# Kernel tuning notes

Hardware: AMD Instinct MI355X
Metric: run time of the kernel (lower is better)

Reference implementation:

```python
import jax, jax.numpy as jnp
import numpy as np

H = 32  # hidden_size from LSTMConfig

def setup_inputs() -> dict:
    key = jax.random.key(0)
    ks = jax.random.split(key, 7)
    B, T, F = 131072, 22, 12
    s = 1.0 / np.sqrt(H)
    return {
        "x": jax.random.normal(ks[0], (B, T, F), dtype=jnp.float32),
        "W_ih": jax.random.uniform(ks[1], (4 * H, F), minval=-s, maxval=s, dtype=jnp.float32),
        "W_hh": jax.random.uniform(ks[2], (4 * H, H), minval=-s, maxval=s, dtype=jnp.float32),
        "b_ih": jax.random.uniform(ks[3], (4 * H,), minval=-s, maxval=s, dtype=jnp.float32),
        "b_hh": jax.random.uniform(ks[4], (4 * H,), minval=-s, maxval=s, dtype=jnp.float32),
        "W_head": jax.random.uniform(ks[5], (1, H), minval=-s, maxval=s, dtype=jnp.float32),
        "b_head": jax.random.uniform(ks[6], (1,), minval=-s, maxval=s, dtype=jnp.float32),
    }

def _lstm_last_hidden(x, W_ih, W_hh, b_ih, b_hh):
    B, T, F = x.shape
    # precompute input contribution for all timesteps: [T, B, 4H]
    gx = jnp.einsum('btf,gf->tbg', x, W_ih) + (b_ih + b_hh)

    def step(carry, gx_t):
        h, c = carry
        g = gx_t + h @ W_hh.T                      # [B, 4H]
        i, f, gg, o = jnp.split(g, 4, axis=-1)     # PyTorch gate order i,f,g,o
        i = jax.nn.sigmoid(i)
        f = jax.nn.sigmoid(f)
        gg = jnp.tanh(gg)
        o = jax.nn.sigmoid(o)
        c = f * c + i * gg
        h = o * jnp.tanh(c)
        return (h, c), None

    h0 = jnp.zeros((B, H), dtype=x.dtype)
    (h, _), _ = jax.lax.scan(step, (h0, h0), gx)
    return h  # [B, H] last timestep hidden

def reference(x, W_ih, W_hh, b_ih, b_hh, W_head, b_head):
    h = _lstm_last_hidden(x, W_ih, W_hh, b_ih, b_hh)
    # Dropout p=0.0 is identity; Linear(H,1) + Softplus, then squeeze(-1)
    y = h @ W_head.T + b_head                      # [B, 1]
    return jax.nn.softplus(y)[:, 0]                # [B]
```

## Files before the change

### kernel.cpp

```cpp
#include <hip/hip_runtime.h>
#include <math.h>

#define T_STEPS 22
#define F_IN    12
#define HID     32

typedef __attribute__((ext_vector_type(8))) short  bf16x8;
typedef __attribute__((ext_vector_type(4)))  float f32x4;
typedef __attribute__((ext_vector_type(2)))  float f32x2;

union FragU { unsigned int u[4]; bf16x8 v; };

#define LOG2E    1.442695041f
#define TWOLOG2E 2.885390082f

static __device__ __forceinline__ unsigned short f2bf(float x) {
    unsigned int u = __builtin_bit_cast(unsigned int, x);
    return (unsigned short)((u + 0x7fffu + ((u >> 16) & 1u)) >> 16);
}

static __device__ __forceinline__ unsigned cvt_pk_bf16(float lo, float hi) {
    unsigned r;
    asm("v_cvt_pk_bf16_f32 %0, %1, %2" : "=v"(r) : "v"(lo), "v"(hi));
    return r;
}

__global__ void prep_kernel(const float* __restrict__ Wih, const float* __restrict__ Whh,
                            const float* __restrict__ bih, const float* __restrict__ bhh,
                            const float* __restrict__ Whead, float* __restrict__ ws) {
    const int tid = threadIdx.x;
    unsigned short* wx = (unsigned short*)ws;
    unsigned short* wh = (unsigned short*)(ws + 2048);
    float* whd = ws + 4096;

    for (int e = tid; e < 512; e += 256) {
        int tile = e >> 6, lane = e & 63;
        int row = lane & 15, s = lane >> 4;
        int g = 16 * tile + row;
        float scale = (tile == 4 || tile == 5) ? TWOLOG2E : -LOG2E;
        for (int j = 0; j < 8; ++j) {
            int k = 8 * s + j;
            float v = 0.0f;
            if (k < F_IN)       v = Wih[g * F_IN + k];
            else if (k == F_IN) v = bih[g] + bhh[g];
            wx[e * 8 + j] = f2bf(scale * v);
            int cc = (j < 4) ? (4 * s + j) : (16 + 4 * s + (j - 4));
            wh[e * 8 + j] = f2bf(scale * Whh[g * HID + cc]);
        }
    }
    if (tid < 32) {
        int s = tid >> 3, j = tid & 7;
        int orig = (j < 4) ? (4 * s + j) : (16 + 4 * s + (j - 4));
        whd[tid] = Whead[orig];
    }
}

__global__ void __launch_bounds__(256, 2)
lstm_kernel(const float* __restrict__ x, const float* __restrict__ ws,
            const float* __restrict__ bheadp, float* __restrict__ out, int B) {
    const int tid  = threadIdx.x;
    const int lane = tid & 63;
    const int wave = tid >> 6;
    const int col  = lane & 15;
    const int s    = lane >> 4;
    int b = blockIdx.x * 64 + wave * 16 + col;
    const bool valid = (b < B);
    if (b >= B) b = B - 1;

    __shared__ float wlds[4096];
#pragma unroll
    for (int i = 0; i < 4; ++i)
        ((float4*)wlds)[tid + i * 256] = ((const float4*)ws)[tid + i * 256];
    __syncthreads();

    const bf16x8* wx_l = (const bf16x8*)wlds;
    const bf16x8* wh_l = ((const bf16x8*)wlds) + 512;

    const float* xr  = x + (size_t)b * (T_STEPS * F_IN);
    const float* xa  = xr + ((s == 0) ? 0 : 8);
    const float* xbp = xr + ((s == 0) ? 4 : 8);

    f32x2 cc[4], hv[4];
#pragma unroll
    for (int q = 0; q < 4; ++q) { cc[q] = (f32x2){0.f, 0.f}; hv[q] = (f32x2){0.f, 0.f}; }
    bf16x8 hf;
#pragma unroll
    for (int j = 0; j < 8; ++j) hf[j] = 0;

    f32x4 zc;
#pragma unroll
    for (int q = 0; q < 4; ++q) zc[q] = 0.0f;

#pragma unroll 1
    for (int t = 0; t < T_STEPS; ++t) {
        asm volatile("" ::: "memory");

        float4 va = *(const float4*)(xa  + t * F_IN);
        float4 vb = *(const float4*)(xbp + t * F_IN);
        unsigned p0 = cvt_pk_bf16(va.x, va.y);
        unsigned p1 = cvt_pk_bf16(va.z, va.w);
        unsigned p2 = cvt_pk_bf16(vb.x, vb.y);
        unsigned p3 = cvt_pk_bf16(vb.z, vb.w);
        FragU xf;
        if (s == 0)      { xf.u[0] = p0; xf.u[1] = p1; xf.u[2] = p2;          xf.u[3] = p3; }
        else if (s == 1) { xf.u[0] = p0; xf.u[1] = p1; xf.u[2] = 0x00003f80u; xf.u[3] = 0;  }
        else             { xf.u[0] = 0;  xf.u[1] = 0;  xf.u[2] = 0;           xf.u[3] = 0;  }

        f32x4 a0, a1, a2, a3, a4, a5, a6, a7;
        a0 = __builtin_amdgcn_mfma_f32_16x16x32_bf16(wx_l[0 * 64 + lane], xf.v, zc, 0, 0, 0);
        a1 = __builtin_amdgcn_mfma_f32_16x16x32_bf16(wx_l[1 * 64 + lane], xf.v, zc, 0, 0, 0);
        a2 = __builtin_amdgcn_mfma_f32_16x16x32_bf16(wx_l[2 * 64 + lane], xf.v, zc, 0, 0, 0);
        a3 = __builtin_amdgcn_mfma_f32_16x16x32_bf16(wx_l[3 * 64 + lane], xf.v, zc, 0, 0, 0);
        a4 = __builtin_amdgcn_mfma_f32_16x16x32_bf16(wx_l[4 * 64 + lane], xf.v, zc, 0, 0, 0);
        a5 = __builtin_amdgcn_mfma_f32_16x16x32_bf16(wx_l[5 * 64 + lane], xf.v, zc, 0, 0, 0);
        a6 = __builtin_amdgcn_mfma_f32_16x16x32_bf16(wx_l[6 * 64 + lane], xf.v, zc, 0, 0, 0);
        a7 = __builtin_amdgcn_mfma_f32_16x16x32_bf16(wx_l[7 * 64 + lane], xf.v, zc, 0, 0, 0);
        a0 = __builtin_amdgcn_mfma_f32_16x16x32_bf16(wh_l[0 * 64 + lane], hf, a0, 0, 0, 0);
        a1 = __builtin_amdgcn_mfma_f32_16x16x32_bf16(wh_l[1 * 64 + lane], hf, a1, 0, 0, 0);
        a2 = __builtin_amdgcn_mfma_f32_16x16x32_bf16(wh_l[2 * 64 + lane], hf, a2, 0, 0, 0);
        a3 = __builtin_amdgcn_mfma_f32_16x16x32_bf16(wh_l[3 * 64 + lane], hf, a3, 0, 0, 0);
        a4 = __builtin_amdgcn_mfma_f32_16x16x32_bf16(wh_l[4 * 64 + lane], hf, a4, 0, 0, 0);
        a5 = __builtin_amdgcn_mfma_f32_16x16x32_bf16(wh_l[5 * 64 + lane], hf, a5, 0, 0, 0);
        a6 = __builtin_amdgcn_mfma_f32_16x16x32_bf16(wh_l[6 * 64 + lane], hf, a6, 0, 0, 0);
        a7 = __builtin_amdgcn_mfma_f32_16x16x32_bf16(wh_l[7 * 64 + lane], hf, a7, 0, 0, 0);
        __builtin_amdgcn_sched_group_barrier(0x100, 8, 0);
        __builtin_amdgcn_sched_group_barrier(0x008, 8, 0);
        __builtin_amdgcn_sched_group_barrier(0x100, 8, 0);
        __builtin_amdgcn_sched_group_barrier(0x008, 8, 0);

        const f32x2 one2 = {1.0f, 1.0f};
#pragma unroll
        for (int q = 0; q < 4; ++q) {
            f32x2 ei = {__builtin_amdgcn_exp2f(a0[q]), __builtin_amdgcn_exp2f(a1[q])};
            f32x2 ef = {__builtin_amdgcn_exp2f(a2[q]), __builtin_amdgcn_exp2f(a3[q])};
            f32x2 eg = {__builtin_amdgcn_exp2f(a4[q]), __builtin_amdgcn_exp2f(a5[q])};
            f32x2 eo = {__builtin_amdgcn_exp2f(a6[q]), __builtin_amdgcn_exp2f(a7[q])};
            f32x2 A  = (one2 + ei) * (one2 + eg);
            f32x2 F  = one2 + ef;
            f32x2 FA = F * A;
            f32x2 r1 = {__builtin_amdgcn_rcpf(FA.x), __builtin_amdgcn_rcpf(FA.y)};
            f32x2 t2 = eg * (f32x2){TWOLOG2E, TWOLOG2E} - (f32x2){TWOLOG2E, TWOLOG2E};
            f32x2 num = t2 * F + cc[q] * A;
            cc[q] = num * r1;
            f32x2 ec = {__builtin_amdgcn_exp2f(cc[q].x), __builtin_amdgcn_exp2f(cc[q].y)};
            f32x2 r2in = (one2 + eo) * (one2 + ec);
            f32x2 r2 = {__builtin_amdgcn_rcpf(r2in.x), __builtin_amdgcn_rcpf(r2in.y)};
            hv[q] = (ec - one2) * r2;
        }

        FragU hh;
        hh.u[0] = cvt_pk_bf16(hv[0].x, hv[1].x);
        hh.u[1] = cvt_pk_bf16(hv[2].x, hv[3].x);
        hh.u[2] = cvt_pk_bf16(hv[0].y, hv[1].y);
        hh.u[3] = cvt_pk_bf16(hv[2].y, hv[3].y);
        hf = hh.v;
    }

    const float* whd = ws + 4096 + s * 8;
    float y = 0.0f;
#pragma unroll
    for (int j = 0; j < 4; ++j) {
        y = fmaf(hv[j].x, whd[j],     y);
        y = fmaf(hv[j].y, whd[4 + j], y);
    }
    y += __shfl_xor(y, 16, 64);
    y += __shfl_xor(y, 32, 64);
    y += bheadp[0];
    float sp = fmaxf(y, 0.0f) + log1pf(expf(-fabsf(y)));
    if (valid && s == 0) out[b] = sp;
}

extern "C" void kernel_launch(void* const* d_in, const int* in_sizes, int n_in,
                              void* d_out, int out_size, void* d_ws, size_t ws_size,
                              hipStream_t stream) {
    const float* x     = (const float*)d_in[0];
    const float* Wih   = (const float*)d_in[1];
    const float* Whh   = (const float*)d_in[2];
    const float* bih   = (const float*)d_in[3];
    const float* bhh   = (const float*)d_in[4];
    const float* Whead = (const float*)d_in[5];
    const float* bhead = (const float*)d_in[6];
    float* out = (float*)d_out;
    float* ws  = (float*)d_ws;

    const int B = in_sizes[0] / (T_STEPS * F_IN);
    const int blocks = (B + 63) / 64;

    hipLaunchKernelGGL(prep_kernel, dim3(1), dim3(256), 0, stream,
                       Wih, Whh, bih, bhh, Whead, ws);
    hipLaunchKernelGGL(lstm_kernel, dim3(blocks), dim3(256), 0, stream,
                       x, ws, bhead, out, B);
}
```

Measured before the change: 103.4 us.

## Interleave two independent batch tiles per wave to hide MFMA and transcendental latency

Each wave now processes two 16-sample tiles, with two independent recurrence chains whose MFMA and exp/rcp work can overlap. Block size in samples doubles, so the grid is halved. Launch bounds are raised to 4 waves per SIMD. The sched_group_barrier hints are removed, and the head projection now reads the bf16-rounded hidden state instead of the fp32 values. This adds register pressure and a slight change in precision at the output.

```diff
diff --git a/kernel.cpp b/kernel.cpp
--- a/kernel.cpp
+++ b/kernel.cpp
@@ -23,6 +23,10 @@
     unsigned r;
     asm("v_cvt_pk_bf16_f32 %0, %1, %2" : "=v"(r) : "v"(lo), "v"(hi));
     return r;
+}
+
+static __device__ __forceinline__ float bf2f(short s_) {
+    return __builtin_bit_cast(float, ((unsigned)(unsigned short)s_) << 16);
 }
 
 __global__ void prep_kernel(const float* __restrict__ Wih, const float* __restrict__ Whh,
@@ -50,12 +54,13 @@
     }
     if (tid < 32) {
         int s = tid >> 3, j = tid & 7;
-        int orig = (j < 4) ? (4 * s + j) : (16 + 4 * s + (j - 4));
+        int orig = (j < 4) ? (4 * s + j) : (16 + 4 * s + (j - 8) + 4);
+        orig = (j < 4) ? (4 * s + j) : (16 + 4 * s + (j - 4));
         whd[tid] = Whead[orig];
     }
 }
 
-__global__ void __launch_bounds__(256, 2)
+__global__ void __launch_bounds__(256, 4)
 lstm_kernel(const float* __restrict__ x, const float* __restrict__ ws,
             const float* __restrict__ bheadp, float* __restrict__ out, int B) {
     const int tid  = threadIdx.x;
@@ -63,9 +68,12 @@
     const int wave = tid >> 6;
     const int col  = lane & 15;
     const int s    = lane >> 4;
-    int b = blockIdx.x * 64 + wave * 16 + col;
-    const bool valid = (b < B);
-    if (b >= B) b = B - 1;
+    const int base = blockIdx.x * 128 + wave * 32;
+    int b0 = base + col;
+    int b1 = base + 16 + col;
+    const bool v0 = (b0 < B), v1 = (b1 < B);
+    if (b0 >= B) b0 = B - 1;
+    if (b1 >= B) b1 = B - 1;
 
     __shared__ float wlds[4096];
 #pragma unroll
@@ -73,101 +81,168 @@
         ((float4*)wlds)[tid + i * 256] = ((const float4*)ws)[tid + i * 256];
     __syncthreads();
 
-    const bf16x8* wx_l = (const bf16x8*)wlds;
-    const bf16x8* wh_l = ((const bf16x8*)wlds) + 512;
-
-    const float* xr  = x + (size_t)b * (T_STEPS * F_IN);
-    const float* xa  = xr + ((s == 0) ? 0 : 8);
-    const float* xbp = xr + ((s == 0) ? 4 : 8);
-
-    f32x2 cc[4], hv[4];
-#pragma unroll
-    for (int q = 0; q < 4; ++q) { cc[q] = (f32x2){0.f, 0.f}; hv[q] = (f32x2){0.f, 0.f}; }
-    bf16x8 hf;
-#pragma unroll
-    for (int j = 0; j < 8; ++j) hf[j] = 0;
+    const int off1 = (s == 0) ? 0 : 8;
+    const int off2 = (s == 0) ? 4 : 8;
+    const float* xa0 = x + (size_t)b0 * (T_STEPS * F_IN) + off1;
+    const float* xb0 = x + (size_t)b0 * (T_STEPS * F_IN) + off2;
+    const float* xa1 = x + (size_t)b1 * (T_STEPS * F_IN) + off1;
+    const float* xb1 = x + (size_t)b1 * (T_STEPS * F_IN) + off2;
+
+    f32x2 cA[4], cB[4];
+#pragma unroll
+    for (int q = 0; q < 4; ++q) { cA[q] = (f32x2){0.f, 0.f}; cB[q] = (f32x2){0.f, 0.f}; }
+    bf16x8 hfA, hfB;
+#pragma unroll
+    for (int j = 0; j < 8; ++j) { hfA[j] = 0; hfB[j] = 0; }
 
     f32x4 zc;
 #pragma unroll
     for (int q = 0; q < 4; ++q) zc[q] = 0.0f;
+
+    const f32x2 one2 = {1.0f, 1.0f};
 
 #pragma unroll 1
     for (int t = 0; t < T_STEPS; ++t) {
-        asm volatile("" ::: "memory");
-
-        float4 va = *(const float4*)(xa  + t * F_IN);
-        float4 vb = *(const float4*)(xbp + t * F_IN);
-        unsigned p0 = cvt_pk_bf16(va.x, va.y);
-        unsigned p1 = cvt_pk_bf16(va.z, va.w);
-        unsigned p2 = cvt_pk_bf16(vb.x, vb.y);
-        unsigned p3 = cvt_pk_bf16(vb.z, vb.w);
-        FragU xf;
-        if (s == 0)      { xf.u[0] = p0; xf.u[1] = p1; xf.u[2] = p2;          xf.u[3] = p3; }
-        else if (s == 1) { xf.u[0] = p0; xf.u[1] = p1; xf.u[2] = 0x00003f80u; xf.u[3] = 0;  }
-        else             { xf.u[0] = 0;  xf.u[1] = 0;  xf.u[2] = 0;           xf.u[3] = 0;  }
-
-        f32x4 a0, a1, a2, a3, a4, a5, a6, a7;
-        a0 = __builtin_amdgcn_mfma_f32_16x16x32_bf16(wx_l[0 * 64 + lane], xf.v, zc, 0, 0, 0);
-        a1 = __builtin_amdgcn_mfma_f32_16x16x32_bf16(wx_l[1 * 64 + lane], xf.v, zc, 0, 0, 0);
-        a2 = __builtin_amdgcn_mfma_f32_16x16x32_bf16(wx_l[2 * 64 + lane], xf.v, zc, 0, 0, 0);
-        a3 = __builtin_amdgcn_mfma_f32_16x16x32_bf16(wx_l[3 * 64 + lane], xf.v, zc, 0, 0, 0);
-        a4 = __builtin_amdgcn_mfma_f32_16x16x32_bf16(wx_l[4 * 64 + lane], xf.v, zc, 0, 0, 0);
-        a5 = __builtin_amdgcn_mfma_f32_16x16x32_bf16(wx_l[5 * 64 + lane], xf.v, zc, 0, 0, 0);
-        a6 = __builtin_amdgcn_mfma_f32_16x16x32_bf16(wx_l[6 * 64 + lane], xf.v, zc, 0, 0, 0);
-        a7 = __builtin_amdgcn_mfma_f32_16x16x32_bf16(wx_l[7 * 64 + lane], xf.v, zc, 0, 0, 0);
-        a0 = __builtin_amdgcn_mfma_f32_16x16x32_bf16(wh_l[0 * 64 + lane], hf, a0, 0, 0, 0);
-        a1 = __builtin_amdgcn_mfma_f32_16x16x32_bf16(wh_l[1 * 64 + lane], hf, a1, 0, 0, 0);
-        a2 = __builtin_amdgcn_mfma_f32_16x16x32_bf16(wh_l[2 * 64 + lane], hf, a2, 0, 0, 0);
-        a3 = __builtin_amdgcn_mfma_f32_16x16x32_bf16(wh_l[3 * 64 + lane], hf, a3, 0, 0, 0);
-        a4 = __builtin_amdgcn_mfma_f32_16x16x32_bf16(wh_l[4 * 64 + lane], hf, a4, 0, 0, 0);
-        a5 = __builtin_amdgcn_mfma_f32_16x16x32_bf16(wh_l[5 * 64 + lane], hf, a5, 0, 0, 0);
-        a6 = __builtin_amdgcn_mfma_f32_16x16x32_bf16(wh_l[6 * 64 + lane], hf, a6, 0, 0, 0);
-        a7 = __builtin_amdgcn_mfma_f32_16x16x32_bf16(wh_l[7 * 64 + lane], hf, a7, 0, 0, 0);
-        __builtin_amdgcn_sched_group_barrier(0x100, 8, 0);
-        __builtin_amdgcn_sched_group_barrier(0x008, 8, 0);
-        __builtin_amdgcn_sched_group_barrier(0x100, 8, 0);
-        __builtin_amdgcn_sched_group_barrier(0x008, 8, 0);
-
-        const f32x2 one2 = {1.0f, 1.0f};
-#pragma unroll
-        for (int q = 0; q < 4; ++q) {
-            f32x2 ei = {__builtin_amdgcn_exp2f(a0[q]), __builtin_amdgcn_exp2f(a1[q])};
-            f32x2 ef = {__builtin_amdgcn_exp2f(a2[q]), __builtin_amdgcn_exp2f(a3[q])};
-            f32x2 eg = {__builtin_amdgcn_exp2f(a4[q]), __builtin_amdgcn_exp2f(a5[q])};
-            f32x2 eo = {__builtin_amdgcn_exp2f(a6[q]), __builtin_amdgcn_exp2f(a7[q])};
-            f32x2 A  = (one2 + ei) * (one2 + eg);
-            f32x2 F  = one2 + ef;
-            f32x2 FA = F * A;
-            f32x2 r1 = {__builtin_amdgcn_rcpf(FA.x), __builtin_amdgcn_rcpf(FA.y)};
-            f32x2 t2 = eg * (f32x2){TWOLOG2E, TWOLOG2E} - (f32x2){TWOLOG2E, TWOLOG2E};
-            f32x2 num = t2 * F + cc[q] * A;
-            cc[q] = num * r1;
-            f32x2 ec = {__builtin_amdgcn_exp2f(cc[q].x), __builtin_amdgcn_exp2f(cc[q].y)};
-            f32x2 r2in = (one2 + eo) * (one2 + ec);
-            f32x2 r2 = {__builtin_amdgcn_rcpf(r2in.x), __builtin_amdgcn_rcpf(r2in.y)};
-            hv[q] = (ec - one2) * r2;
-        }
-
-        FragU hh;
-        hh.u[0] = cvt_pk_bf16(hv[0].x, hv[1].x);
-        hh.u[1] = cvt_pk_bf16(hv[2].x, hv[3].x);
-        hh.u[2] = cvt_pk_bf16(hv[0].y, hv[1].y);
-        hh.u[3] = cvt_pk_bf16(hv[2].y, hv[3].y);
-        hf = hh.v;
+        int zr = 0;
+        asm("" : "+v"(zr));
+        const bf16x8* wx_l = ((const bf16x8*)wlds) + zr;
+        const bf16x8* wh_l = ((const bf16x8*)wlds) + 512 + zr;
+
+        float4 vaA = *(const float4*)(xa0 + t * F_IN);
+        float4 vbA = *(const float4*)(xb0 + t * F_IN);
+        float4 vaB = *(const float4*)(xa1 + t * F_IN);
+        float4 vbB = *(const float4*)(xb1 + t * F_IN);
+
+        FragU xfA, xfB;
+        {
+            unsigned p0 = cvt_pk_bf16(vaA.x, vaA.y);
+            unsigned p1 = cvt_pk_bf16(vaA.z, vaA.w);
+            unsigned p2 = cvt_pk_bf16(vbA.x, vbA.y);
+            unsigned p3 = cvt_pk_bf16(vbA.z, vbA.w);
+            if (s == 0)      { xfA.u[0] = p0; xfA.u[1] = p1; xfA.u[2] = p2;          xfA.u[3] = p3; }
+            else if (s == 1) { xfA.u[0] = p0; xfA.u[1] = p1; xfA.u[2] = 0x00003f80u; xfA.u[3] = 0;  }
+            else             { xfA.u[0] = 0;  xfA.u[1] = 0;  xfA.u[2] = 0;           xfA.u[3] = 0;  }
+        }
+        {
+            unsigned p0 = cvt_pk_bf16(vaB.x, vaB.y);
+            unsigned p1 = cvt_pk_bf16(vaB.z, vaB.w);
+            unsigned p2 = cvt_pk_bf16(vbB.x, vbB.y);
+            unsigned p3 = cvt_pk_bf16(vbB.z, vbB.w);
+            if (s == 0)      { xfB.u[0] = p0; xfB.u[1] = p1; xfB.u[2] = p2;          xfB.u[3] = p3; }
+            else if (s == 1) { xfB.u[0] = p0; xfB.u[1] = p1; xfB.u[2] = 0x00003f80u; xfB.u[3] = 0;  }
+            else             { xfB.u[0] = 0;  xfB.u[1] = 0;  xfB.u[2] = 0;           xfB.u[3] = 0;  }
+        }
+
+        f32x4 aA0, aA1, aA2, aA3, aA4, aA5, aA6, aA7;
+        aA0 = __builtin_amdgcn_mfma_f32_16x16x32_bf16(wx_l[0 * 64 + lane], xfA.v, zc, 0, 0, 0);
+        aA1 = __builtin_amdgcn_mfma_f32_16x16x32_bf16(wx_l[1 * 64 + lane], xfA.v, zc, 0, 0, 0);
+        aA2 = __builtin_amdgcn_mfma_f32_16x16x32_bf16(wx_l[2 * 64 + lane], xfA.v, zc, 0, 0, 0);
+        aA3 = __builtin_amdgcn_mfma_f32_16x16x32_bf16(wx_l[3 * 64 + lane], xfA.v, zc, 0, 0, 0);
+        aA4 = __builtin_amdgcn_mfma_f32_16x16x32_bf16(wx_l[4 * 64 + lane], xfA.v, zc, 0, 0, 0);
+        aA5 = __builtin_amdgcn_mfma_f32_16x16x32_bf16(wx_l[5 * 64 + lane], xfA.v, zc, 0, 0, 0);
+        aA6 = __builtin_amdgcn_mfma_f32_16x16x32_bf16(wx_l[6 * 64 + lane], xfA.v, zc, 0, 0, 0);
+        aA7 = __builtin_amdgcn_mfma_f32_16x16x32_bf16(wx_l[7 * 64 + lane], xfA.v, zc, 0, 0, 0);
+        aA0 = __builtin_amdgcn_mfma_f32_16x16x32_bf16(wh_l[0 * 64 + lane], hfA, aA0, 0, 0, 0);
+        aA1 = __builtin_amdgcn_mfma_f32_16x16x32_bf16(wh_l[1 * 64 + lane], hfA, aA1, 0, 0, 0);
+        aA2 = __builtin_amdgcn_mfma_f32_16x16x32_bf16(wh_l[2 * 64 + lane], hfA, aA2, 0, 0, 0);
+        aA3 = __builtin_amdgcn_mfma_f32_16x16x32_bf16(wh_l[3 * 64 + lane], hfA, aA3, 0, 0, 0);
+        aA4 = __builtin_amdgcn_mfma_f32_16x16x32_bf16(wh_l[4 * 64 + lane], hfA, aA4, 0, 0, 0);
+        aA5 = __builtin_amdgcn_mfma_f32_16x16x32_bf16(wh_l[5 * 64 + lane], hfA, aA5, 0, 0, 0);
+        aA6 = __builtin_amdgcn_mfma_f32_16x16x32_bf16(wh_l[6 * 64 + lane], hfA, aA6, 0, 0, 0);
+        aA7 = __builtin_amdgcn_mfma_f32_16x16x32_bf16(wh_l[7 * 64 + lane], hfA, aA7, 0, 0, 0);
+
+        f32x4 aB0, aB1, aB2, aB3, aB4, aB5, aB6, aB7;
+        aB0 = __builtin_amdgcn_mfma_f32_16x16x32_bf16(wx_l[0 * 64 + lane], xfB.v, zc, 0, 0, 0);
+        aB1 = __builtin_amdgcn_mfma_f32_16x16x32_bf16(wx_l[1 * 64 + lane], xfB.v, zc, 0, 0, 0);
+        aB2 = __builtin_amdgcn_mfma_f32_16x16x32_bf16(wx_l[2 * 64 + lane], xfB.v, zc, 0, 0, 0);
+        aB3 = __builtin_amdgcn_mfma_f32_16x16x32_bf16(wx_l[3 * 64 + lane], xfB.v, zc, 0, 0, 0);
+        aB4 = __builtin_amdgcn_mfma_f32_16x16x32_bf16(wx_l[4 * 64 + lane], xfB.v, zc, 0, 0, 0);
+        aB5 = __builtin_amdgcn_mfma_f32_16x16x32_bf16(wx_l[5 * 64 + lane], xfB.v, zc, 0, 0, 0);
+        aB6 = __builtin_amdgcn_mfma_f32_16x16x32_bf16(wx_l[6 * 64 + lane], xfB.v, zc, 0, 0, 0);
+        aB7 = __builtin_amdgcn_mfma_f32_16x16x32_bf16(wx_l[7 * 64 + lane], xfB.v, zc, 0, 0, 0);
+        aB0 = __builtin_amdgcn_mfma_f32_16x16x32_bf16(wh_l[0 * 64 + lane], hfB, aB0, 0, 0, 0);
+        aB1 = __builtin_amdgcn_mfma_f32_16x16x32_bf16(wh_l[1 * 64 + lane], hfB, aB1, 0, 0, 0);
+        aB2 = __builtin_amdgcn_mfma_f32_16x16x32_bf16(wh_l[2 * 64 + lane], hfB, aB2, 0, 0, 0);
+        aB3 = __builtin_amdgcn_mfma_f32_16x16x32_bf16(wh_l[3 * 64 + lane], hfB, aB3, 0, 0, 0);
+        aB4 = __builtin_amdgcn_mfma_f32_16x16x32_bf16(wh_l[4 * 64 + lane], hfB, aB4, 0, 0, 0);
+        aB5 = __builtin_amdgcn_mfma_f32_16x16x32_bf16(wh_l[5 * 64 + lane], hfB, aB5, 0, 0, 0);
+        aB6 = __builtin_amdgcn_mfma_f32_16x16x32_bf16(wh_l[6 * 64 + lane], hfB, aB6, 0, 0, 0);
+        aB7 = __builtin_amdgcn_mfma_f32_16x16x32_bf16(wh_l[7 * 64 + lane], hfB, aB7, 0, 0, 0);
+
+        {
+            f32x2 hv[4];
+#pragma unroll
+            for (int q = 0; q < 4; ++q) {
+                f32x2 ei = {__builtin_amdgcn_exp2f(aA0[q]), __builtin_amdgcn_exp2f(aA1[q])};
+                f32x2 ef = {__builtin_amdgcn_exp2f(aA2[q]), __builtin_amdgcn_exp2f(aA3[q])};
+                f32x2 eg = {__builtin_amdgcn_exp2f(aA4[q]), __builtin_amdgcn_exp2f(aA5[q])};
+                f32x2 eo = {__builtin_amdgcn_exp2f(aA6[q]), __builtin_amdgcn_exp2f(aA7[q])};
+                f32x2 A  = (one2 + ei) * (one2 + eg);
+                f32x2 F  = one2 + ef;
+                f32x2 FA = F * A;
+                f32x2 r1 = {__builtin_amdgcn_rcpf(FA.x), __builtin_amdgcn_rcpf(FA.y)};
+                f32x2 t2 = eg * (f32x2){TWOLOG2E, TWOLOG2E} - (f32x2){TWOLOG2E, TWOLOG2E};
+                f32x2 num = t2 * F + cA[q] * A;
+                cA[q] = num * r1;
+                f32x2 ec = {__builtin_amdgcn_exp2f(cA[q].x), __builtin_amdgcn_exp2f(cA[q].y)};
+                f32x2 r2in = (one2 + eo) * (one2 + ec);
+                f32x2 r2 = {__builtin_amdgcn_rcpf(r2in.x), __builtin_amdgcn_rcpf(r2in.y)};
+                hv[q] = (ec - one2) * r2;
+            }
+            FragU hh;
+            hh.u[0] = cvt_pk_bf16(hv[0].x, hv[1].x);
+            hh.u[1] = cvt_pk_bf16(hv[2].x, hv[3].x);
+            hh.u[2] = cvt_pk_bf16(hv[0].y, hv[1].y);
+            hh.u[3] = cvt_pk_bf16(hv[2].y, hv[3].y);
+            hfA = hh.v;
+        }
+        {
+            f32x2 hv[4];
+#pragma unroll
+            for (int q = 0; q < 4; ++q) {
+                f32x2 ei = {__builtin_amdgcn_exp2f(aB0[q]), __builtin_amdgcn_exp2f(aB1[q])};
+                f32x2 ef = {__builtin_amdgcn_exp2f(aB2[q]), __builtin_amdgcn_exp2f(aB3[q])};
+                f32x2 eg = {__builtin_amdgcn_exp2f(aB4[q]), __builtin_amdgcn_exp2f(aB5[q])};
+                f32x2 eo = {__builtin_amdgcn_exp2f(aB6[q]), __builtin_amdgcn_exp2f(aB7[q])};
+                f32x2 A  = (one2 + ei) * (one2 + eg);
+                f32x2 F  = one2 + ef;
+                f32x2 FA = F * A;
+                f32x2 r1 = {__builtin_amdgcn_rcpf(FA.x), __builtin_amdgcn_rcpf(FA.y)};
+                f32x2 t2 = eg * (f32x2){TWOLOG2E, TWOLOG2E} - (f32x2){TWOLOG2E, TWOLOG2E};
+                f32x2 num = t2 * F + cB[q] * A;
+                cB[q] = num * r1;
+                f32x2 ec = {__builtin_amdgcn_exp2f(cB[q].x), __builtin_amdgcn_exp2f(cB[q].y)};
+                f32x2 r2in = (one2 + eo) * (one2 + ec);
+                f32x2 r2 = {__builtin_amdgcn_rcpf(r2in.x), __builtin_amdgcn_rcpf(r2in.y)};
+                hv[q] = (ec - one2) * r2;
+            }
+            FragU hh;
+            hh.u[0] = cvt_pk_bf16(hv[0].x, hv[1].x);
+            hh.u[1] = cvt_pk_bf16(hv[2].x, hv[3].x);
+            hh.u[2] = cvt_pk_bf16(hv[0].y, hv[1].y);
+            hh.u[3] = cvt_pk_bf16(hv[2].y, hv[3].y);
+            hfB = hh.v;
+        }
     }
 
     const float* whd = ws + 4096 + s * 8;
-    float y = 0.0f;
-#pragma unroll
-    for (int j = 0; j < 4; ++j) {
-        y = fmaf(hv[j].x, whd[j],     y);
-        y = fmaf(hv[j].y, whd[4 + j], y);
-    }
-    y += __shfl_xor(y, 16, 64);
-    y += __shfl_xor(y, 32, 64);
-    y += bheadp[0];
-    float sp = fmaxf(y, 0.0f) + log1pf(expf(-fabsf(y)));
-    if (valid && s == 0) out[b] = sp;
+    float y0 = 0.0f, y1 = 0.0f;
+#pragma unroll
+    for (int e = 0; e < 8; ++e) {
+        y0 = fmaf(bf2f(hfA[e]), whd[e], y0);
+        y1 = fmaf(bf2f(hfB[e]), whd[e], y1);
+    }
+    y0 += __shfl_xor(y0, 16, 64);
+    y0 += __shfl_xor(y0, 32, 64);
+    y1 += __shfl_xor(y1, 16, 64);
+    y1 += __shfl_xor(y1, 32, 64);
+    float bh = bheadp[0];
+    y0 += bh;
+    y1 += bh;
+    float sp0 = fmaxf(y0, 0.0f) + log1pf(expf(-fabsf(y0)));
+    float sp1 = fmaxf(y1, 0.0f) + log1pf(expf(-fabsf(y1)));
+    if (v0 && s == 0) out[b0] = sp0;
+    if (v1 && s == 0) out[b1] = sp1;
 }
 
 extern "C" void kernel_launch(void* const* d_in, const int* in_sizes, int n_in,
@@ -184,7 +259,7 @@
     float* ws  = (float*)d_ws;
 
     const int B = in_sizes[0] / (T_STEPS * F_IN);
-    const int blocks = (B + 63) / 64;
+    const int blocks = (B + 127) / 128;
 
     hipLaunchKernelGGL(prep_kernel, dim3(1), dim3(256), 0, stream,
                        Wih, Whh, bih, bhh, Whead, ws);
```

After: 136.5 us. +32.0%, slower.
